# Performance work log

Hardware: AMD Instinct MI355X
Metric: run time of the kernel (lower is better)

The kernel has to match this reference:

```python
import jax, jax.numpy as jnp
import numpy as np

TEMPERATURE = 0.1
EPS = 1e-12  # F.normalize eps


def setup_inputs() -> dict:
    key = jax.random.key(0)
    k1, k2 = jax.random.split(key)
    B, D = 4096, 128
    return {
        "x_i": jax.random.normal(k1, (B, D), dtype=jnp.float32),
        "x_j": jax.random.normal(k2, (B, D), dtype=jnp.float32),
    }


def _l2_normalize(x):
    n = jnp.sqrt(jnp.sum(x * x, axis=1, keepdims=True))
    return x / jnp.maximum(n, EPS)


def reference(x_i, x_j):
    B = x_i.shape[0]
    z = jnp.concatenate([_l2_normalize(x_i), _l2_normalize(x_j)], axis=0)  # [2B, D]
    # cosine similarity of unit-norm rows == dot product -> single GEMM
    sim = z @ z.T  # [2B, 2B]
    idx = jnp.arange(B)
    sim_ij = sim[idx, idx + B]   # diag(sim, +B)
    sim_ji = sim[idx + B, idx]   # diag(sim, -B)
    positives = jnp.concatenate([sim_ij, sim_ji], axis=0)  # [2B]
    neg_mask = 1.0 - jnp.eye(2 * B, dtype=sim.dtype)
    denominator = jnp.sum(neg_mask * jnp.exp(sim / TEMPERATURE), axis=1)  # [2B]
    # -log(exp(pos/t) / denom) = -(pos/t - log denom)
    loss_partial = jnp.log(denominator) - positives / TEMPERATURE
    return jnp.sum(loss_partial) / (2 * B)
```

## Files before the change

kernel.cpp:

```cpp
#include <hip/hip_runtime.h>
#include <stdint.h>

#define D_DIM 128
#define NROW 8192
#define L2EPS 1e-12f
#define SCALE_A 14.426950408889634f
#define LN2 0.6931471805599453f

typedef __attribute__((ext_vector_type(4))) int   i32x4;
typedef __attribute__((ext_vector_type(8))) int   i32x8;
typedef __attribute__((ext_vector_type(4))) float f32x4;

#define AS1 __attribute__((address_space(1)))
#define AS3 __attribute__((address_space(3)))

static __device__ inline void gload_lds16(const void* g, void* l) {
    __builtin_amdgcn_global_load_lds((const AS1 uint32_t*)g, (AS3 uint32_t*)l, 16, 0, 0);
}

static __device__ inline i32x8 cat8(i32x4 lo, i32x4 hi) {
    i32x8 r;
    r[0] = lo[0]; r[1] = lo[1]; r[2] = lo[2]; r[3] = lo[3];
    r[4] = hi[0]; r[5] = hi[1]; r[6] = hi[2]; r[7] = hi[3];
    return r;
}

__global__ __launch_bounds__(256) void k_normalize(
        const float* __restrict__ xi, const float* __restrict__ xj,
        uint8_t* __restrict__ z8, uint8_t* __restrict__ z8s,
        float* __restrict__ pos_acc, float* __restrict__ logsum) {
    const int wave = threadIdx.x >> 6;
    const int lane = threadIdx.x & 63;
    const int row = blockIdx.x * 4 + wave;
    const float* src = (row < 4096) ? (xi + (size_t)row * D_DIM)
                                    : (xj + (size_t)(row - 4096) * D_DIM);
    float2 v = *(const float2*)(src + lane * 2);
    float ss = v.x * v.x + v.y * v.y;
#pragma unroll
    for (int m = 32; m >= 1; m >>= 1) ss += __shfl_xor(ss, m, 64);
    const float scale = 1.0f / fmaxf(sqrtf(ss), L2EPS);
    const float scale_a = scale * SCALE_A;
    const int pk_b = __builtin_amdgcn_cvt_pk_fp8_f32(v.x * scale,   v.y * scale,   0, false);
    const int pk_a = __builtin_amdgcn_cvt_pk_fp8_f32(v.x * scale_a, v.y * scale_a, 0, false);
    *(ushort*)(z8  + (size_t)row * D_DIM + lane * 2) = (ushort)pk_b;
    *(ushort*)(z8s + (size_t)row * D_DIM + lane * 2) = (ushort)pk_a;

    if (blockIdx.x == 0 && threadIdx.x == 0) { pos_acc[0] = 0.0f; logsum[0] = 0.0f; }
}

__global__ __launch_bounds__(256) void k_gemm(
        const uint8_t* __restrict__ z8, const uint8_t* __restrict__ z8s,
        float* __restrict__ denom_part, float* __restrict__ pos_acc) {
    __shared__ __align__(16) uint8_t lds[32768];

    const int bid = blockIdx.x;
    const int t = threadIdx.x;
    const int wave = t >> 6, lane = t & 63;
    const int quad = lane >> 4, lc = lane & 15;

    const int rb = bid >> 5;
    const int cc = bid & 31;
    const int rowbase = rb * 128;
    const int colbase = cc * 256;

    {
        const uint8_t* zb = z8 + (size_t)colbase * D_DIM;
#pragma unroll
        for (int q = 0; q < 8; q++) {
            const int s = q * 256 + t;
            const int r = s >> 3;
            const int g = (s & 7) ^ (r & 7);
            gload_lds16(zb + (size_t)r * D_DIM + g * 16, &lds[s * 16]);
        }
    }

    i32x8 afr[2];
    {
        const uint8_t* pa = z8s + (size_t)(rowbase + wave * 32 + lc) * D_DIM + quad * 32;
#pragma unroll
        for (int i = 0; i < 2; i++) {
            i32x4 lo = *(const i32x4*)(pa + i * 16 * D_DIM);
            i32x4 hi = *(const i32x4*)(pa + i * 16 * D_DIM + 16);
            afr[i] = cat8(lo, hi);
        }
    }

    asm volatile("s_waitcnt vmcnt(0)" ::: "memory");
    __syncthreads();

    const bool diagblk = (cc == (rb >> 1));
    const int  j0d = (rb & 1) * 8 + wave * 2;
    const int  rbp = rb ^ 32;
    const bool posblk = (cc == (rbp >> 1));
    const int  j0p = (rbp & 1) * 8 + wave * 2;

    float rs[2][4] = {{0.f,0.f,0.f,0.f},{0.f,0.f,0.f,0.f}};
    float posp = 0.f;
    const int rgbase = rowbase + wave * 32 + quad * 4;

#pragma unroll 4
    for (int j = 0; j < 16; j++) {
        const int rowb = (j * 16 + lc) * D_DIM;
        i32x4 blo = *(const i32x4*)&lds[rowb + (((quad * 2)     ^ (lc & 7)) * 16)];
        i32x4 bhi = *(const i32x4*)&lds[rowb + (((quad * 2 + 1) ^ (lc & 7)) * 16)];
        const i32x8 bfr = cat8(blo, bhi);

        f32x4 z4 = {0.f, 0.f, 0.f, 0.f};
        f32x4 a0 = __builtin_amdgcn_mfma_scale_f32_16x16x128_f8f6f4(
                       afr[0], bfr, z4, 0, 0, 0, 127, 0, 127);
        f32x4 a1 = __builtin_amdgcn_mfma_scale_f32_16x16x128_f8f6f4(
                       afr[1], bfr, z4, 0, 0, 0, 127, 0, 127);

        const bool careful = (diagblk && (unsigned)(j - j0d) < 2u) ||
                             (posblk  && (unsigned)(j - j0p) < 2u);
        if (careful) {
            const int cg = colbase + j * 16 + lc;
#pragma unroll
            for (int i = 0; i < 2; i++) {
#pragma unroll
                for (int r = 0; r < 4; r++) {
                    const float s = (i ? a1 : a0)[r];
                    float e = exp2f(s);
                    const int rg = rgbase + i * 16 + r;
                    if (rg == cg) e = 0.f;
                    if (cg == (rg ^ 4096)) posp += s;
                    rs[i][r] += e;
                }
            }
        } else {
#pragma unroll
            for (int r = 0; r < 4; r++) {
                rs[0][r] += exp2f(a0[r]);
                rs[1][r] += exp2f(a1[r]);
            }
        }
    }

#pragma unroll
    for (int i = 0; i < 2; i++)
#pragma unroll
        for (int r = 0; r < 4; r++) {
            float v = rs[i][r];
            v += __shfl_xor(v, 1, 64);
            v += __shfl_xor(v, 2, 64);
            v += __shfl_xor(v, 4, 64);
            v += __shfl_xor(v, 8, 64);
            if (lc == 0)
                denom_part[(size_t)cc * NROW + rgbase + i * 16 + r] = v;
        }

    if (posblk) {
#pragma unroll
        for (int m = 32; m >= 1; m >>= 1) posp += __shfl_xor(posp, m, 64);
        if (lane == 0) atomicAdd(pos_acc, posp);
    }
}

__global__ __launch_bounds__(256) void k_logsum(
        const float* __restrict__ denom_part, float* __restrict__ logsum) {
    const int row = blockIdx.x * 256 + threadIdx.x;
    float d = 0.f;
#pragma unroll
    for (int p = 0; p < 32; p++) d += denom_part[(size_t)p * NROW + row];
    float v = __logf(d);
#pragma unroll
    for (int m = 32; m >= 1; m >>= 1) v += __shfl_xor(v, m, 64);
    if ((threadIdx.x & 63) == 0) atomicAdd(logsum, v);
}

__global__ void k_combine(const float* __restrict__ logsum,
                          const float* __restrict__ pos_acc,
                          float* __restrict__ out) {
    out[0] = (logsum[0] - pos_acc[0] * LN2) / (float)NROW;
}

extern "C" void kernel_launch(void* const* d_in, const int* in_sizes, int n_in,
                              void* d_out, int out_size, void* d_ws, size_t ws_size,
                              hipStream_t stream) {
    const float* xi = (const float*)d_in[0];
    const float* xj = (const float*)d_in[1];
    uint8_t* z8  = (uint8_t*)d_ws;
    uint8_t* z8s = z8 + (size_t)NROW * D_DIM;
    float* denom_part = (float*)(z8s + (size_t)NROW * D_DIM);
    float* pos_acc = denom_part + 32 * NROW;
    float* logsum = pos_acc + 1;
    float* out = (float*)d_out;

    hipLaunchKernelGGL(k_normalize, dim3(NROW / 4), dim3(256), 0, stream,
                       xi, xj, z8, z8s, pos_acc, logsum);
    hipLaunchKernelGGL(k_gemm, dim3(2048), dim3(256), 0, stream,
                       z8, z8s, denom_part, pos_acc);
    hipLaunchKernelGGL(k_logsum, dim3(NROW / 256), dim3(256), 0, stream,
                       denom_part, logsum);
    hipLaunchKernelGGL(k_combine, dim3(1), dim3(1), 0, stream,
                       logsum, pos_acc, out);
}
```

Baseline: 86.41 us.

## Exploit similarity matrix symmetry: compute upper-triangular tiles with row and column sums

Only the upper triangle of the symmetric similarity matrix is computed, which cuts the GEMM grid from 2048 to 1056 blocks. Each block also accumulates column sums of exp values, reduced through LDS into an extra 64 partial slabs, so the lower-triangle contributions are recovered. Positives are taken from a single side and doubled. The cost is the column-reduction work and LDS syncs per block, a zeroing pass over a larger workspace, and a logsum kernel that reads 96 partials instead of 32. The asymmetric fp8 scaling of A versus B assumes the scaled products are symmetric.

```diff
diff --git a/kernel.cpp b/kernel.cpp
--- a/kernel.cpp
+++ b/kernel.cpp
@@ -6,6 +6,7 @@
 #define L2EPS 1e-12f
 #define SCALE_A 14.426950408889634f
 #define LN2 0.6931471805599453f
+#define NPART 96
 
 typedef __attribute__((ext_vector_type(4))) int   i32x4;
 typedef __attribute__((ext_vector_type(8))) int   i32x8;
@@ -28,7 +29,8 @@
 __global__ __launch_bounds__(256) void k_normalize(
         const float* __restrict__ xi, const float* __restrict__ xj,
         uint8_t* __restrict__ z8, uint8_t* __restrict__ z8s,
-        float* __restrict__ pos_acc, float* __restrict__ logsum) {
+        float* __restrict__ part, float* __restrict__ pos_acc,
+        float* __restrict__ logsum) {
     const int wave = threadIdx.x >> 6;
     const int lane = threadIdx.x & 63;
     const int row = blockIdx.x * 4 + wave;
@@ -45,21 +47,27 @@
     *(ushort*)(z8  + (size_t)row * D_DIM + lane * 2) = (ushort)pk_b;
     *(ushort*)(z8s + (size_t)row * D_DIM + lane * 2) = (ushort)pk_a;
 
+    const int tid = blockIdx.x * 256 + threadIdx.x;
+#pragma unroll
+    for (int k = 0; k < 2; k++) {
+        const int idx = tid + k * (2048 * 256);
+        if (idx < NPART * NROW) part[idx] = 0.0f;
+    }
     if (blockIdx.x == 0 && threadIdx.x == 0) { pos_acc[0] = 0.0f; logsum[0] = 0.0f; }
 }
 
 __global__ __launch_bounds__(256) void k_gemm(
         const uint8_t* __restrict__ z8, const uint8_t* __restrict__ z8s,
-        float* __restrict__ denom_part, float* __restrict__ pos_acc) {
+        float* __restrict__ part, float* __restrict__ pos_acc) {
     __shared__ __align__(16) uint8_t lds[32768];
 
-    const int bid = blockIdx.x;
     const int t = threadIdx.x;
     const int wave = t >> 6, lane = t & 63;
     const int quad = lane >> 4, lc = lane & 15;
 
-    const int rb = bid >> 5;
-    const int cc = bid & 31;
+    int rem = blockIdx.x, rb = 0;
+    while (rem >= 32 - (rb >> 1)) { rem -= 32 - (rb >> 1); rb++; }
+    const int cc = (rb >> 1) + rem;
     const int rowbase = rb * 128;
     const int colbase = cc * 256;
 
@@ -89,17 +97,21 @@
     __syncthreads();
 
     const bool diagblk = (cc == (rb >> 1));
-    const int  j0d = (rb & 1) * 8 + wave * 2;
-    const int  rbp = rb ^ 32;
-    const bool posblk = (cc == (rbp >> 1));
-    const int  j0p = (rbp & 1) * 8 + wave * 2;
+    const int  jd_lo = (rb & 1) ? 8 : 0;
+    const bool posblk = (rb < 32) && (cc == 16 + (rb >> 1));
+    const int  j0p = (rb & 1) * 8 + wave * 2;
 
     float rs[2][4] = {{0.f,0.f,0.f,0.f},{0.f,0.f,0.f,0.f}};
+    float cs[16];
+#pragma unroll
+    for (int j = 0; j < 16; j++) cs[j] = 0.f;
     float posp = 0.f;
     const int rgbase = rowbase + wave * 32 + quad * 4;
 
-#pragma unroll 4
+#pragma unroll
     for (int j = 0; j < 16; j++) {
+        if (diagblk && (rb & 1) && j < 8) continue;
+
         const int rowb = (j * 16 + lc) * D_DIM;
         i32x4 blo = *(const i32x4*)&lds[rowb + (((quad * 2)     ^ (lc & 7)) * 16)];
         i32x4 bhi = *(const i32x4*)&lds[rowb + (((quad * 2 + 1) ^ (lc & 7)) * 16)];
@@ -111,27 +123,39 @@
         f32x4 a1 = __builtin_amdgcn_mfma_scale_f32_16x16x128_f8f6f4(
                        afr[1], bfr, z4, 0, 0, 0, 127, 0, 127);
 
-        const bool careful = (diagblk && (unsigned)(j - j0d) < 2u) ||
-                             (posblk  && (unsigned)(j - j0p) < 2u);
-        if (careful) {
+        if (diagblk && j >= jd_lo && j < jd_lo + 8) {
             const int cg = colbase + j * 16 + lc;
 #pragma unroll
-            for (int i = 0; i < 2; i++) {
+            for (int i = 0; i < 2; i++)
 #pragma unroll
                 for (int r = 0; r < 4; r++) {
                     const float s = (i ? a1 : a0)[r];
-                    float e = exp2f(s);
                     const int rg = rgbase + i * 16 + r;
-                    if (rg == cg) e = 0.f;
-                    if (cg == (rg ^ 4096)) posp += s;
+                    const float e = (cg > rg) ? exp2f(s) : 0.f;
                     rs[i][r] += e;
+                    cs[j] += e;
                 }
-            }
+        } else if (posblk && (unsigned)(j - j0p) < 2u) {
+            const int cg = colbase + j * 16 + lc;
+#pragma unroll
+            for (int i = 0; i < 2; i++)
+#pragma unroll
+                for (int r = 0; r < 4; r++) {
+                    const float s = (i ? a1 : a0)[r];
+                    const float e = exp2f(s);
+                    const int rg = rgbase + i * 16 + r;
+                    if (cg == rg + 4096) posp += s;
+                    rs[i][r] += e;
+                    cs[j] += e;
+                }
         } else {
 #pragma unroll
             for (int r = 0; r < 4; r++) {
-                rs[0][r] += exp2f(a0[r]);
-                rs[1][r] += exp2f(a1[r]);
+                const float e0 = exp2f(a0[r]);
+                const float e1 = exp2f(a1[r]);
+                rs[0][r] += e0;
+                rs[1][r] += e1;
+                cs[j] += e0 + e1;
             }
         }
     }
@@ -146,8 +170,26 @@
             v += __shfl_xor(v, 4, 64);
             v += __shfl_xor(v, 8, 64);
             if (lc == 0)
-                denom_part[(size_t)cc * NROW + rgbase + i * 16 + r] = v;
-        }
+                part[(size_t)cc * NROW + rgbase + i * 16 + r] = v;
+        }
+
+#pragma unroll
+    for (int j = 0; j < 16; j++) {
+        cs[j] += __shfl_xor(cs[j], 16, 64);
+        cs[j] += __shfl_xor(cs[j], 32, 64);
+    }
+    __syncthreads();
+    float* colred = (float*)lds;
+    if (quad == 0) {
+#pragma unroll
+        for (int j = 0; j < 16; j++)
+            colred[wave * 256 + j * 16 + lc] = cs[j];
+    }
+    __syncthreads();
+    if (t < 256) {
+        const float v = colred[t] + colred[256 + t] + colred[512 + t] + colred[768 + t];
+        part[(size_t)(32 + rb) * NROW + colbase + t] = v;
+    }
 
     if (posblk) {
 #pragma unroll
@@ -157,11 +199,11 @@
 }
 
 __global__ __launch_bounds__(256) void k_logsum(
-        const float* __restrict__ denom_part, float* __restrict__ logsum) {
+        const float* __restrict__ part, float* __restrict__ logsum) {
     const int row = blockIdx.x * 256 + threadIdx.x;
     float d = 0.f;
 #pragma unroll
-    for (int p = 0; p < 32; p++) d += denom_part[(size_t)p * NROW + row];
+    for (int p = 0; p < NPART; p++) d += part[(size_t)p * NROW + row];
     float v = __logf(d);
 #pragma unroll
     for (int m = 32; m >= 1; m >>= 1) v += __shfl_xor(v, m, 64);
@@ -171,7 +213,7 @@
 __global__ void k_combine(const float* __restrict__ logsum,
                           const float* __restrict__ pos_acc,
                           float* __restrict__ out) {
-    out[0] = (logsum[0] - pos_acc[0] * LN2) / (float)NROW;
+    out[0] = (logsum[0] - pos_acc[0] * 2.0f * LN2) / (float)NROW;
 }
 
 extern "C" void kernel_launch(void* const* d_in, const int* in_sizes, int n_in,
@@ -181,17 +223,17 @@
     const float* xj = (const float*)d_in[1];
     uint8_t* z8  = (uint8_t*)d_ws;
     uint8_t* z8s = z8 + (size_t)NROW * D_DIM;
-    float* denom_part = (float*)(z8s + (size_t)NROW * D_DIM);
-    float* pos_acc = denom_part + 32 * NROW;
+    float* part = (float*)(z8s + (size_t)NROW * D_DIM);
+    float* pos_acc = part + (size_t)NPART * NROW;
     float* logsum = pos_acc + 1;
     float* out = (float*)d_out;
 
     hipLaunchKernelGGL(k_normalize, dim3(NROW / 4), dim3(256), 0, stream,
-                       xi, xj, z8, z8s, pos_acc, logsum);
-    hipLaunchKernelGGL(k_gemm, dim3(2048), dim3(256), 0, stream,
-                       z8, z8s, denom_part, pos_acc);
+                       xi, xj, z8, z8s, part, pos_acc, logsum);
+    hipLaunchKernelGGL(k_gemm, dim3(1056), dim3(256), 0, stream,
+                       z8, z8s, part, pos_acc);
     hipLaunchKernelGGL(k_logsum, dim3(NROW / 256), dim3(256), 0, stream,
-                       denom_part, logsum);
+                       part, logsum);
     hipLaunchKernelGGL(k_combine, dim3(1), dim3(1), 0, stream,
                        logsum, pos_acc, out);
 }
```

Result: slower. 109.4 us (+26.6%).
